# Kernel optimization log

Hardware: AMD Instinct MI355X
Metric: run time of the kernel (lower is better)

The kernel has to match this reference:

```python
import jax, jax.numpy as jnp
import numpy as np

NUM_HEADS = 8
EPS = 1e-6


def hamilton(a, b):
    # Quaternion (Hamilton) product on the last axis (size 4), broadcasting leading dims.
    aw, ax, ay, az = a[..., 0], a[..., 1], a[..., 2], a[..., 3]
    bw, bx, by, bz = b[..., 0], b[..., 1], b[..., 2], b[..., 3]
    return jnp.stack([
        aw * bw - ax * bx - ay * by - az * bz,
        aw * bx + ax * bw + ay * bz - az * by,
        aw * by - ax * bz + ay * bw + az * bx,
        aw * bz + ax * by - ay * bx + az * bw,
    ], axis=-1)


def setup_inputs() -> dict:
    key = jax.random.key(0)
    ks = jax.random.split(key, 7)
    B, L, E = 2, 384, 512
    s = 1.0 / np.sqrt(E)
    return {
        'x': jax.random.normal(ks[0], (B, L, E), dtype=jnp.float32),
        'Wq': jax.random.normal(ks[1], (E, E), dtype=jnp.float32) * s,
        'Wk': jax.random.normal(ks[2], (E, E), dtype=jnp.float32) * s,
        'Wv': jax.random.normal(ks[3], (E, E), dtype=jnp.float32) * s,
        'Wo': jax.random.normal(ks[4], (E, E), dtype=jnp.float32) * s,
        'dde_w': jax.random.normal(ks[5], (4, 4), dtype=jnp.float32) * 0.5,
        'dde_b': jnp.zeros((4,), dtype=jnp.float32),
    }


def reference(x, Wq, Wk, Wv, Wo, dde_w, dde_b):
    B, L, E = x.shape
    H = NUM_HEADS
    hd = E // H            # head_dim
    c = hd // 4            # quaternion atoms per head

    def proj_quat(W):
        # x @ W^T  -> split heads -> quaternion atoms: (B*H, L, c, 4)
        y = jnp.einsum('ble,fe->blf', x, W)
        y = y.reshape(B, L, H, hd).transpose(0, 2, 1, 3)  # (B,H,L,hd)
        return y.reshape(B * H, L, c, 4)

    q = proj_quat(Wq)
    k = proj_quat(Wk)
    v = proj_quat(Wv)

    # Broadcasted Hamilton product: (BH, L, L, c, 4)
    interference = hamilton(q[:, :, None, :, :], k[:, None, :, :, :])
    norm = jnp.linalg.norm(interference, axis=-1, keepdims=True) + EPS
    spinor = interference / norm

    # Discrete decision gate: mean over atoms -> (BH, L, L, 4) -> sigmoid(linear)
    gate_in = spinor.mean(axis=-2)
    gate = jax.nn.sigmoid(jnp.einsum('blmq,pq->blmp', gate_in, dde_w) + dde_b)
    spinor = spinor * gate[:, :, :, None, :]

    # Value aggregation: Hamilton product with v, summed over key positions j
    ctx = hamilton(spinor, v[:, None, :, :, :]).sum(axis=2)  # (BH, L, c, 4)

    ctx = ctx.reshape(B, H, L, hd).transpose(0, 2, 1, 3).reshape(B, L, E)
    return jnp.einsum('ble,fe->blf', ctx, Wo)
```

## Files before the change

kernel.cpp:

```cpp
#include <hip/hip_runtime.h>
#include <math.h>

#define L_SEQ 384
#define E_DIM 512
#define NHEAD 8
#define NBH   16
#define HD    64
#define LOG2E 1.44269504f

typedef __attribute__((ext_vector_type(8))) __bf16 bf16x8;
typedef __attribute__((ext_vector_type(8))) _Float16 f16x8;
typedef __attribute__((ext_vector_type(4))) float f32x4;

union u4h8 { uint4 u; f16x8 h; };

__device__ __forceinline__ float uniform_f(float v) {
  return __uint_as_float(__builtin_amdgcn_readfirstlane(__float_as_uint(v)));
}

__device__ __forceinline__ unsigned f2bf(float f) {
  unsigned u = __float_as_uint(f);
  return (u + 0x7FFFu + ((u >> 16) & 1u)) >> 16;
}

__device__ __forceinline__ unsigned ror16(unsigned x) { return (x >> 16) | (x << 16); }

__device__ __forceinline__ float dpp_xor1(float x) {
  return __int_as_float(__builtin_amdgcn_mov_dpp(__float_as_int(x), 0xB1, 0xF, 0xF, 0));
}
__device__ __forceinline__ float dpp_xor2(float x) {
  return __int_as_float(__builtin_amdgcn_mov_dpp(__float_as_int(x), 0x4E, 0xF, 0xF, 0));
}
template <int IMM>
__device__ __forceinline__ float swz_xor(float x) {
  return __int_as_float(__builtin_amdgcn_ds_swizzle(__float_as_int(x), IMM));
}

__device__ __forceinline__ size_t pidx(int row, int k, int Kd) {
  return ((((size_t)(row >> 4) * (Kd >> 5) + (k >> 5)) * 4 + ((k >> 3) & 3)) * 16
          + (row & 15)) * 8 + (k & 7);
}

__global__ __launch_bounds__(256) void to_bf16_all(
    const float* __restrict__ x, const float* __restrict__ Wq,
    const float* __restrict__ Wk, const float* __restrict__ Wv,
    const float* __restrict__ Wo, unsigned short* __restrict__ dst1,
    unsigned short* __restrict__ dst2, float* __restrict__ outz)
{
  int e0 = (blockIdx.x * 256 + threadIdx.x) * 4;
  if (e0 >= 1835008) return;
  if (e0 >= 1441792) {
    *(float4*)(outz + (e0 - 1441792)) = make_float4(0.f, 0.f, 0.f, 0.f);
    return;
  }
  const float* src; unsigned short* d; int s;
  if (e0 < 393216)       { src = x;  s = e0;           d = dst1; }
  else if (e0 < 655360)  { src = Wq; s = e0 - 393216;  d = dst1 + 393216; }
  else if (e0 < 917504)  { src = Wk; s = e0 - 655360;  d = dst1 + 655360; }
  else if (e0 < 1179648) { src = Wv; s = e0 - 917504;  d = dst1 + 917504; }
  else                   { src = Wo; s = e0 - 1179648; d = dst2; }
  float4 v = *(const float4*)(src + s);
  unsigned lo = f2bf(v.x) | (f2bf(v.y) << 16);
  unsigned hi = f2bf(v.z) | (f2bf(v.w) << 16);
  int row = s >> 9, k = s & 511;
  *(uint2*)(d + pidx(row, k, 512)) = make_uint2(lo, hi);
}

template <int NTN, int MODE>
__global__ __launch_bounds__(256) void gemm_mfma(
    const __bf16* __restrict__ A, const __bf16* __restrict__ B0,
    const __bf16* __restrict__ B1, const __bf16* __restrict__ B2,
    float* __restrict__ C0, float* __restrict__ C1, float* __restrict__ C2,
    int M, int N, int K)
{
  const int z = blockIdx.z;
  const __bf16* Bm = (MODE == 2) ? B0 : (z == 0) ? B0 : (z == 1) ? B1 : B2;
  float* Cp = (MODE == 2) ? C0 : (z == 0) ? C0 : (z == 1) ? C1 : C2;

  const int tid = threadIdx.x;
  const int wave = tid >> 6, lane = tid & 63;
  const int m0 = blockIdx.y * 64 + wave * 16;
  const int n0 = blockIdx.x * (16 * NTN);
  const int mr = lane & 15, quad = lane >> 4;
  const int KT = K >> 5;
  const int kb0 = (MODE == 2) ? z * 4 : 0;
  const int KL = (MODE == 2) ? 4 : KT;

  f32x4 acc[NTN];
  #pragma unroll
  for (int nt = 0; nt < NTN; ++nt) acc[nt] = (f32x4){0.f, 0.f, 0.f, 0.f};

  const __bf16* ap = A + ((size_t)(m0 >> 4) * KT + kb0) * 512 + lane * 8;
  const __bf16* bp = Bm + ((size_t)(n0 >> 4) * KT + kb0) * 512 + lane * 8;

  #pragma unroll 4
  for (int ks = 0; ks < KL; ++ks) {
    bf16x8 a = *(const bf16x8*)(ap + (size_t)ks * 512);
    #pragma unroll
    for (int nt = 0; nt < NTN; ++nt) {
      bf16x8 b = *(const bf16x8*)(bp + ((size_t)nt * KT + ks) * 512);
      acc[nt] = __builtin_amdgcn_mfma_f32_16x16x32_bf16(a, b, acc[nt], 0, 0, 0);
    }
  }

  if (MODE == 2) {
    #pragma unroll
    for (int nt = 0; nt < NTN; ++nt) {
      int n = n0 + nt * 16 + mr;
      #pragma unroll
      for (int r = 0; r < 4; ++r) {
        int m = m0 + quad * 4 + r;
        __hip_atomic_fetch_add(&Cp[(size_t)m * N + n], acc[nt][r],
                               __ATOMIC_RELAXED, __HIP_MEMORY_SCOPE_AGENT);
      }
    }
  } else {
    _Float16* Hp = (_Float16*)Cp;
    #pragma unroll
    for (int nt = 0; nt < NTN; ++nt) {
      int n = n0 + nt * 16 + mr;
      #pragma unroll
      for (int r = 0; r < 4; ++r) {
        float val = acc[nt][r];
        float s = val * val;
        s += dpp_xor1(s);
        s += dpp_xor2(s);
        float sc = (z == 2) ? 1.f : __builtin_amdgcn_rsqf(fmaxf(s, 1e-30f));
        int m = m0 + quad * 4 + r;
        int b = m / L_SEQ, l = m - b * L_SEQ;
        int row = (b * NHEAD + (n >> 6)) * L_SEQ + l;
        Hp[pidx(row, n & 63, 64)] = (_Float16)(val * sc);
      }
    }
  }
}

__global__ __launch_bounds__(256) void z_build(
    const _Float16* __restrict__ khh, const _Float16* __restrict__ vhh,
    _Float16* __restrict__ Z0)
{
  const int tid = threadIdx.x;
  const int l = blockIdx.x * 64 + (tid & 63);
  const int a = blockIdx.y * 4 + (tid >> 6);
  const int bh = blockIdx.z;

  size_t off = pidx(bh * L_SEQ + l, a * 4, 64);
  union { uint2 u; _Float16 h[4]; } kk, vv;
  kk.u = *(const uint2*)(khh + off);
  vv.u = *(const uint2*)(vhh + off);

  float kb[4] = {(float)kk.h[0], (float)kk.h[1], (float)kk.h[2], (float)kk.h[3]};
  float ve[4] = {(float)vv.h[0], (float)vv.h[1], (float)vv.h[2], (float)vv.h[3]};
  _Float16* zp = Z0 + (size_t)bh * (256 * 384);
  #pragma unroll
  for (int b = 0; b < 4; ++b)
    #pragma unroll
    for (int e = 0; e < 4; ++e)
      zp[pidx(a * 16 + b * 4 + e, l, 384)] = (_Float16)(kb[b] * ve[e]);
}

__global__ __launch_bounds__(256) void gate_pv(
    const _Float16* __restrict__ qhh, const _Float16* __restrict__ khh,
    const _Float16* __restrict__ Z0, const float* __restrict__ dde_w,
    const float* __restrict__ dde_b, unsigned short* __restrict__ CTXB)
{
  __shared__ _Float16 gbuf[4096];
  __shared__ float vxs[4][4][16][4];
  __shared__ float qs[16][17];

  const int tid = threadIdx.x, w = tid >> 6, lane = tid & 63;
  const int mr = lane & 15, quad = lane >> 4;
  const int bh = blockIdx.z, cg = blockIdx.y, ib = blockIdx.x;
  const int i0 = ib * 16;

  {
    int il = tid >> 4, t = tid & 15;
    qs[il][t] = (float)qhh[pidx(bh * L_SEQ + i0 + il, cg * 16 + t, 64)];
  }

  float wn[16], bn[4];
  #pragma unroll
  for (int t = 0; t < 16; ++t) wn[t] = uniform_f(dde_w[t]) * (-LOG2E * 0.0625f);
  #pragma unroll
  for (int c = 0; c < 4; ++c) bn[c] = uniform_f(dde_b[c]) * (-LOG2E);

  u4h8 fr[4][2];
  {
    const _Float16* ap = qhh + ((size_t)(bh * 24 + ib)) * 2 * 512 + lane * 8;
    #pragma unroll
    for (int ks = 0; ks < 2; ++ks) {
      uint4 qa = *(const uint4*)(ap + ks * 512);
      unsigned s0 = ror16(qa.x), s1 = ror16(qa.y), s2 = ror16(qa.z), s3 = ror16(qa.w);
      fr[0][ks].u = make_uint4(qa.x ^ 0x80000000u, qa.y ^ 0x80008000u,
                               qa.z ^ 0x80000000u, qa.w ^ 0x80008000u);
      fr[1][ks].u = make_uint4(s0, s1 ^ 0x00008000u, s2, s3 ^ 0x00008000u);
      fr[2][ks].u = make_uint4(qa.y, qa.x ^ 0x80000000u, qa.w, qa.z ^ 0x80000000u);
      fr[3][ks].u = make_uint4(s1 ^ 0x80000000u, s0, s3 ^ 0x80000000u, s2);
    }
  }

  const int bq = mr >> 2, e = mr & 3;
  const unsigned msk =
      ((((0x284Eu >> (w * 4 + bq)) ^ (0xC6A0u >> (w * 4 + e))) & 1u) << 31);

  f32x4 acc[4];
  #pragma unroll
  for (int nt = 0; nt < 4; ++nt) acc[nt] = (f32x4){0.f, 0.f, 0.f, 0.f};

  const int jl = w * 16 + mr;
  const int gw = (jl >> 3) * 128 + (jl & 7) + quad * 32;

  for (int ch = 0; ch < 6; ++ch) {
    u4h8 zb[2][4];
    #pragma unroll
    for (int ks2 = 0; ks2 < 2; ++ks2)
      #pragma unroll
      for (int nt = 0; nt < 4; ++nt)
        zb[ks2][nt].h = *(const f16x8*)(Z0 + (size_t)bh * (256 * 384)
                         + (((size_t)(cg * 4 + nt) * 12 + ch * 2 + ks2) * 512) + lane * 8);

    const _Float16* bp = khh + ((size_t)(bh * 24 + ch * 4 + w)) * 2 * 512 + lane * 8;
    u4h8 kb[2];
    kb[0].h = *(const f16x8*)(bp);
    kb[1].h = *(const f16x8*)(bp + 512);
    f32x4 accS[4];
    #pragma unroll
    for (int c = 0; c < 4; ++c) {
      accS[c] = (f32x4){0.f, 0.f, 0.f, 0.f};
      accS[c] = __builtin_amdgcn_mfma_f32_16x16x32_f16(fr[c][0].h, kb[0].h, accS[c], 0, 0, 0);
      accS[c] = __builtin_amdgcn_mfma_f32_16x16x32_f16(fr[c][1].h, kb[1].h, accS[c], 0, 0, 0);
    }

    #pragma unroll
    for (int r = 0; r < 4; ++r) {
      float S0 = accS[0][r], S1 = accS[1][r], S2 = accS[2][r], S3 = accS[3][r];
      #pragma unroll
      for (int c = 0; c < 4; ++c) {
        float n = bn[c] + wn[c*4+0]*S0 + wn[c*4+1]*S1 + wn[c*4+2]*S2 + wn[c*4+3]*S3;
        float g = __builtin_amdgcn_rcpf(1.f + __builtin_amdgcn_exp2f(n));
        gbuf[c * 1024 + gw + r * 8] = (_Float16)g;
      }
    }
    __syncthreads();

    #pragma unroll
    for (int ks2 = 0; ks2 < 2; ++ks2) {
      f16x8 aa = *(const f16x8*)&gbuf[(w * 2 + ks2) * 512 + lane * 8];
      #pragma unroll
      for (int nt = 0; nt < 4; ++nt)
        acc[nt] = __builtin_amdgcn_mfma_f32_16x16x32_f16(aa, zb[ks2][nt].h, acc[nt], 0, 0, 0);
    }
    __syncthreads();
  }

  #pragma unroll
  for (int nt = 0; nt < 4; ++nt) {
    #pragma unroll
    for (int r = 0; r < 4; ++r) {
      int il = quad * 4 + r;
      float sq = __uint_as_float(__float_as_uint(qs[il][nt * 4 + (bq ^ w)]) ^ msk);
      float v = sq * acc[nt][r];
      v += swz_xor<0x101F>(v);
      v += swz_xor<0x201F>(v);
      if (bq == 0) vxs[w][e][il][nt] = v;
    }
  }
  __syncthreads();

  {
    int il = tid >> 4, cc = tid & 15, nt = cc >> 2, d = cc & 3;
    float s = vxs[0][d][il][nt] + vxs[1][1 ^ d][il][nt] +
              vxs[2][2 ^ d][il][nt] + vxs[3][3 ^ d][il][nt];
    int bb_ = bh >> 3, hh = bh & 7;
    CTXB[pidx(bb_ * L_SEQ + i0 + il, hh * HD + cg * 16 + nt * 4 + d, 512)] =
        (unsigned short)f2bf(s);
  }
}

extern "C" void kernel_launch(void* const* d_in, const int* in_sizes, int n_in,
                              void* d_out, int out_size, void* d_ws, size_t ws_size,
                              hipStream_t stream)
{
  const float* x     = (const float*)d_in[0];
  const float* Wq    = (const float*)d_in[1];
  const float* Wk    = (const float*)d_in[2];
  const float* Wv    = (const float*)d_in[3];
  const float* Wo    = (const float*)d_in[4];
  const float* dde_w = (const float*)d_in[5];
  const float* dde_b = (const float*)d_in[6];
  float* out = (float*)d_out;

  char* ws = (char*)d_ws;
  unsigned short* Wob  = (unsigned short*)(ws + 0);
  _Float16* qhh = (_Float16*)(ws + 524288);
  _Float16* khh = (_Float16*)(ws + 1310720);
  _Float16* Z0h = (_Float16*)(ws + 2097152);
  _Float16* vhh = (_Float16*)(ws + 5242880);
  unsigned short* CTXB = (unsigned short*)(ws + 5242880);
  unsigned short* xb  = (unsigned short*)(ws + 6029312);
  unsigned short* Wqb = (unsigned short*)(ws + 6815744);
  unsigned short* Wkb = (unsigned short*)(ws + 7340032);
  unsigned short* Wvb = (unsigned short*)(ws + 7864320);

  to_bf16_all<<<1792, 256, 0, stream>>>(x, Wq, Wk, Wv, Wo, xb, Wob, out);

  gemm_mfma<1, 1><<<dim3(32, 12, 3), 256, 0, stream>>>(
      (const __bf16*)xb, (const __bf16*)Wqb, (const __bf16*)Wkb, (const __bf16*)Wvb,
      (float*)qhh, (float*)khh, (float*)vhh, 2 * L_SEQ, E_DIM, E_DIM);

  z_build<<<dim3(6, 4, 16), 256, 0, stream>>>(khh, vhh, Z0h);

  gate_pv<<<dim3(24, 4, 16), 256, 0, stream>>>(qhh, khh, Z0h, dde_w, dde_b, CTXB);

  gemm_mfma<2, 2><<<dim3(16, 12, 4), 256, 0, stream>>>(
      (const __bf16*)CTXB, (const __bf16*)Wob, nullptr, nullptr,
      out, nullptr, nullptr, 2 * L_SEQ, E_DIM, E_DIM);
}
```

Measured before the change: 110.1 us.

## Fold column-group grid axis into gate_pv block to reuse gate computation

Removes the cg grid dimension so each block covers all four column groups, one per wave. The gate/sigmoid computation and the score MFMAs therefore run once per (bh, i-tile) rather than four times. The gate buffer is double-buffered so the trailing barrier per chunk can be dropped, and the cross-wave LDS reduction is replaced with in-register DPP shuffles and packed bf16 stores. The cost is a 4x larger accumulator (64 floats) with higher register pressure, and the grid shrinks from 1536 to 384 blocks.

```diff
diff --git a/kernel.cpp b/kernel.cpp
--- a/kernel.cpp
+++ b/kernel.cpp
@@ -164,18 +164,20 @@
     const _Float16* __restrict__ Z0, const float* __restrict__ dde_w,
     const float* __restrict__ dde_b, unsigned short* __restrict__ CTXB)
 {
-  __shared__ _Float16 gbuf[4096];
-  __shared__ float vxs[4][4][16][4];
-  __shared__ float qs[16][17];
+  __shared__ _Float16 gbuf[2][4096];
+  __shared__ float qs[16][65];
 
   const int tid = threadIdx.x, w = tid >> 6, lane = tid & 63;
   const int mr = lane & 15, quad = lane >> 4;
-  const int bh = blockIdx.z, cg = blockIdx.y, ib = blockIdx.x;
+  const int bh = blockIdx.y, ib = blockIdx.x;
   const int i0 = ib * 16;
 
   {
-    int il = tid >> 4, t = tid & 15;
-    qs[il][t] = (float)qhh[pidx(bh * L_SEQ + i0 + il, cg * 16 + t, 64)];
+    int il = tid >> 4, k4 = (tid & 15) * 4;
+    union { uint2 u; _Float16 h[4]; } cv;
+    cv.u = *(const uint2*)(qhh + pidx(bh * L_SEQ + i0 + il, k4, 64));
+    qs[il][k4 + 0] = (float)cv.h[0]; qs[il][k4 + 1] = (float)cv.h[1];
+    qs[il][k4 + 2] = (float)cv.h[2]; qs[il][k4 + 3] = (float)cv.h[3];
   }
 
   float wn[16], bn[4];
@@ -200,16 +202,21 @@
   }
 
   const int bq = mr >> 2, e = mr & 3;
-  const unsigned msk =
-      ((((0x284Eu >> (w * 4 + bq)) ^ (0xC6A0u >> (w * 4 + e))) & 1u) << 31);
-
-  f32x4 acc[4];
-  #pragma unroll
-  for (int nt = 0; nt < 4; ++nt) acc[nt] = (f32x4){0.f, 0.f, 0.f, 0.f};
+  unsigned msk[4];
+  #pragma unroll
+  for (int c = 0; c < 4; ++c)
+    msk[c] = ((((0x284Eu >> (c * 4 + bq)) ^ (0xC6A0u >> (c * 4 + e))) & 1u) << 31);
+
+  f32x4 acc[4][4];
+  #pragma unroll
+  for (int c = 0; c < 4; ++c)
+    #pragma unroll
+    for (int nt = 0; nt < 4; ++nt) acc[c][nt] = (f32x4){0.f, 0.f, 0.f, 0.f};
 
   const int jl = w * 16 + mr;
   const int gw = (jl >> 3) * 128 + (jl & 7) + quad * 32;
 
+  #pragma unroll 2
   for (int ch = 0; ch < 6; ++ch) {
     u4h8 zb[2][4];
     #pragma unroll
@@ -217,7 +224,7 @@
       #pragma unroll
       for (int nt = 0; nt < 4; ++nt)
         zb[ks2][nt].h = *(const f16x8*)(Z0 + (size_t)bh * (256 * 384)
-                         + (((size_t)(cg * 4 + nt) * 12 + ch * 2 + ks2) * 512) + lane * 8);
+                         + (((size_t)(w * 4 + nt) * 12 + ch * 2 + ks2) * 512) + lane * 8);
 
     const _Float16* bp = khh + ((size_t)(bh * 24 + ch * 4 + w)) * 2 * 512 + lane * 8;
     u4h8 kb[2];
@@ -238,42 +245,54 @@
       for (int c = 0; c < 4; ++c) {
         float n = bn[c] + wn[c*4+0]*S0 + wn[c*4+1]*S1 + wn[c*4+2]*S2 + wn[c*4+3]*S3;
         float g = __builtin_amdgcn_rcpf(1.f + __builtin_amdgcn_exp2f(n));
-        gbuf[c * 1024 + gw + r * 8] = (_Float16)g;
+        gbuf[ch & 1][c * 1024 + gw + r * 8] = (_Float16)g;
       }
     }
     __syncthreads();
 
     #pragma unroll
     for (int ks2 = 0; ks2 < 2; ++ks2) {
-      f16x8 aa = *(const f16x8*)&gbuf[(w * 2 + ks2) * 512 + lane * 8];
-      #pragma unroll
-      for (int nt = 0; nt < 4; ++nt)
-        acc[nt] = __builtin_amdgcn_mfma_f32_16x16x32_f16(aa, zb[ks2][nt].h, acc[nt], 0, 0, 0);
-    }
-    __syncthreads();
-  }
-
+      #pragma unroll
+      for (int c = 0; c < 4; ++c) {
+        f16x8 aa = *(const f16x8*)&gbuf[ch & 1][c * 1024 + ks2 * 512 + lane * 8];
+        #pragma unroll
+        for (int nt = 0; nt < 4; ++nt)
+          acc[c][nt] = __builtin_amdgcn_mfma_f32_16x16x32_f16(aa, zb[ks2][nt].h, acc[c][nt], 0, 0, 0);
+      }
+    }
+  }
+
+  const int bb_ = bh >> 3, hh = bh & 7;
   #pragma unroll
   for (int nt = 0; nt < 4; ++nt) {
     #pragma unroll
     for (int r = 0; r < 4; ++r) {
       int il = quad * 4 + r;
-      float sq = __uint_as_float(__float_as_uint(qs[il][nt * 4 + (bq ^ w)]) ^ msk);
-      float v = sq * acc[nt][r];
-      v += swz_xor<0x101F>(v);
-      v += swz_xor<0x201F>(v);
-      if (bq == 0) vxs[w][e][il][nt] = v;
-    }
-  }
-  __syncthreads();
-
-  {
-    int il = tid >> 4, cc = tid & 15, nt = cc >> 2, d = cc & 3;
-    float s = vxs[0][d][il][nt] + vxs[1][1 ^ d][il][nt] +
-              vxs[2][2 ^ d][il][nt] + vxs[3][3 ^ d][il][nt];
-    int bb_ = bh >> 3, hh = bh & 7;
-    CTXB[pidx(bb_ * L_SEQ + i0 + il, hh * HD + cg * 16 + nt * 4 + d, 512)] =
-        (unsigned short)f2bf(s);
+      float pb[4];
+      #pragma unroll
+      for (int c = 0; c < 4; ++c) {
+        float sq = __uint_as_float(
+            __float_as_uint(qs[il][w * 16 + nt * 4 + (bq ^ c)]) ^ msk[c]);
+        float v = sq * acc[c][nt][r];
+        v += swz_xor<0x101F>(v);
+        v += swz_xor<0x201F>(v);
+        pb[c] = v;
+      }
+      float q0 = pb[0] + dpp_xor1(pb[1]);
+      float q1 = pb[1] + dpp_xor1(pb[0]);
+      float q2 = pb[2] + dpp_xor1(pb[3]);
+      float q3 = pb[3] + dpp_xor1(pb[2]);
+      float r0 = q0 + dpp_xor2(q2);
+      float r1 = q1 + dpp_xor2(q3);
+      float r2 = q2 + dpp_xor2(q0);
+      float r3 = q3 + dpp_xor2(q1);
+      if (mr == 0) {
+        unsigned lo = f2bf(r0) | (f2bf(r1) << 16);
+        unsigned hi = f2bf(r2) | (f2bf(r3) << 16);
+        *(uint2*)&CTXB[pidx(bb_ * L_SEQ + i0 + il,
+                            hh * HD + w * 16 + nt * 4, 512)] = make_uint2(lo, hi);
+      }
+    }
   }
 }
 
@@ -310,7 +329,7 @@
 
   z_build<<<dim3(6, 4, 16), 256, 0, stream>>>(khh, vhh, Z0h);
 
-  gate_pv<<<dim3(24, 4, 16), 256, 0, stream>>>(qhh, khh, Z0h, dde_w, dde_b, CTXB);
+  gate_pv<<<dim3(24, 16), 256, 0, stream>>>(qhh, khh, Z0h, dde_w, dde_b, CTXB);
 
   gemm_mfma<2, 2><<<dim3(16, 12, 4), 256, 0, stream>>>(
       (const __bf16*)CTXB, (const __bf16*)Wob, nullptr, nullptr,
```

New measurement: 102.8 us. 6.6% less time.
